# Kernel optimization log

Hardware: AMD Instinct MI355X
Metric: run time of the kernel (lower is better)

## Reference

```python
import jax, jax.numpy as jnp
import numpy as np

N_HOPS = 3
GAMMA = 0.2
N_CAP = 3  # self.N: hops < N use alpha, hop == N uses eta
EPS = 1e-8

N_USERS, N_ENT, N_KG_EDGES, N_INTER_EDGES, D, N_REL = 50000, 100000, 300000, 300000, 256, 21


def setup_inputs() -> dict:
    key = jax.random.key(0)
    ks = jax.random.split(key, 9)
    user_emb = jax.random.normal(ks[0], (N_USERS, D), jnp.float32) * 0.1
    entity_emb = jax.random.normal(ks[1], (N_ENT, D), jnp.float32) * 0.1
    edge_index = jax.random.randint(ks[2], (2, N_KG_EDGES), 0, N_ENT, dtype=jnp.int32)
    edge_type = jax.random.randint(ks[3], (N_KG_EDGES,), 1, N_REL, dtype=jnp.int32)  # 1-based relation ids
    omega = jax.random.uniform(ks[4], (N_KG_EDGES,), jnp.float32)
    inter_u = jax.random.randint(ks[5], (N_INTER_EDGES,), 0, N_USERS, dtype=jnp.int32)
    inter_i = jax.random.randint(ks[6], (N_INTER_EDGES,), 0, N_ENT, dtype=jnp.int32)
    inter_edge = jnp.stack([inter_u, inter_i])
    inter_edge_w = jax.random.uniform(ks[7], (N_INTER_EDGES,), jnp.float32)
    relation_emb = jax.random.normal(ks[8], (N_REL - 1, D), jnp.float32) * 0.1  # xavier-like
    return {
        "user_emb": user_emb,
        "entity_emb": entity_emb,
        "edge_index": edge_index,
        "edge_type": edge_type,
        "omega": omega,
        "inter_edge": inter_edge,
        "inter_edge_w": inter_edge_w,
        "relation_emb": relation_emb,
    }


def _l2norm(x):
    # F.normalize(x, dim=-1, eps=1e-8): x / max(||x||_2, eps)
    n = jnp.sqrt(jnp.sum(x * x, axis=-1, keepdims=True))
    return x / jnp.maximum(n, EPS)


def _clean(x):
    return jnp.nan_to_num(x, nan=0.0, posinf=10000.0, neginf=0.0001)


def reference(user_emb, entity_emb, edge_index, edge_type, omega, inter_edge, inter_edge_w, relation_emb):
    head, tail = edge_index[0], edge_index[1]
    E = omega.shape[0]
    n_ent = entity_emb.shape[0]
    n_users = user_emb.shape[0]

    # alpha/eta depend only on omega & head (constant across hops) -> hoist out of the hop loop
    denom = jax.ops.segment_sum(omega, head, num_segments=E)[head] + EPS
    alpha = omega / denom
    eta0 = jnp.where(alpha > GAMMA, alpha, 0.0)
    eta = eta0 / (jax.ops.segment_sum(eta0, head, num_segments=E)[head] + EPS)

    rel = relation_emb[edge_type - 1]  # [E, D]
    cnt = jnp.maximum(jax.ops.segment_sum(jnp.ones((E,), entity_emb.dtype), head, num_segments=n_ent), 1.0)

    ent_res, usr_res = entity_emb, user_emb
    ent, usr = entity_emb, user_emb
    for i in range(N_HOPS):
        hop = i + 1
        rho = alpha if hop < N_CAP else eta
        msg = rho[:, None] * (ent[tail] * rel)                       # [E, D]
        ent_agg = jax.ops.segment_sum(msg, head, num_segments=n_ent) / cnt[:, None]  # scatter_mean
        item_agg = inter_edge_w[:, None] * ent[inter_edge[1]]        # [IE, D]
        usr_agg = jax.ops.segment_sum(item_agg, inter_edge[0], num_segments=n_users)  # scatter_sum
        ent = _clean(_l2norm(ent_agg))
        usr = _clean(_l2norm(usr_agg))
        ent_res = ent_res + ent
        usr_res = usr_res + usr
    return (ent_res, usr_res)
```

## Files before the change

### kernel.cpp

```cpp
#include <hip/hip_runtime.h>
#include <math.h>

#define D 256
#define EPSV 1e-8f
#define GAMMAV 0.2f
#define SCAN_B 256

typedef float f32x2 __attribute__((ext_vector_type(2)));

__device__ __forceinline__ float cleanf(float x) {
    if (isnan(x)) return 0.0f;
    if (isinf(x)) return x > 0.0f ? 10000.0f : 0.0001f;
    return x;
}

__device__ __forceinline__ unsigned short f2bf(float x) {
    unsigned u = __float_as_uint(x);
    return (unsigned short)((u + 0x7FFFu + ((u >> 16) & 1u)) >> 16);
}
__device__ __forceinline__ float bf2f(unsigned short b) {
    return __uint_as_float(((unsigned)b) << 16);
}

__device__ __forceinline__ float ewgt(int bits, bool eta, float den2i) {
    float a = __int_as_float(bits);
    return eta ? ((a > GAMMAV) ? a * den2i : 0.0f) : a;
}

__device__ __forceinline__ f32x2 bfpair(unsigned u) {
    f32x2 p;
    p.x = __uint_as_float(u << 16);
    p.y = __uint_as_float(u & 0xFFFF0000u);
    return p;
}

__device__ __forceinline__ void pk_wfma(f32x2& acc, f32x2 w2, f32x2 e, f32x2 r) {
    f32x2 t;
    asm("v_pk_mul_f32 %0, %1, %2" : "=v"(t) : "v"(e), "v"(r));
    asm("v_pk_fma_f32 %0, %1, %2, %0" : "+v"(acc) : "v"(w2), "v"(t));
}
__device__ __forceinline__ void pk_wadd(f32x2& acc, f32x2 w2, f32x2 e) {
    asm("v_pk_fma_f32 %0, %1, %2, %0" : "+v"(acc) : "v"(w2), "v"(e));
}


__global__ __launch_bounds__(256) void k_pre(
    const float4* __restrict__ ein, ushort4* __restrict__ eout, int n4, int nbc,
    const int* __restrict__ head, const float* __restrict__ omega,
    const int* __restrict__ iu,
    int* __restrict__ counts_e, int* __restrict__ counts_u,
    float* __restrict__ denom, int E, int IE) {
    if ((int)blockIdx.x < nbc) {
        int i = blockIdx.x * 256 + threadIdx.x;
        if (i < n4) {
            float4 v = ein[i];
            eout[i] = make_ushort4(f2bf(v.x), f2bf(v.y), f2bf(v.z), f2bf(v.w));
        }
    } else {
        int i = (blockIdx.x - nbc) * 256 + threadIdx.x;
        if (i < E) {
            int h = head[i];
            atomicAdd(&counts_e[h], 1);
            atomicAdd(&denom[h], omega[i]);
        } else if (i < E + IE) {
            atomicAdd(&counts_u[iu[i - E]], 1);
        }
    }
}


__global__ __launch_bounds__(SCAN_B) void k_scan1(
    const int* __restrict__ ce, int* __restrict__ oe, int* __restrict__ be,
    int nE, int nbE,
    const int* __restrict__ cu, int* __restrict__ ou, int* __restrict__ bu,
    int nU) {
    __shared__ int tmp[SCAN_B];
    const int* in; int* out; int* bs; int n; int lb;
    if ((int)blockIdx.x < nbE) { in = ce; out = oe; bs = be; n = nE; lb = blockIdx.x; }
    else { in = cu; out = ou; bs = bu; n = nU; lb = blockIdx.x - nbE; }
    int i = lb * SCAN_B + threadIdx.x;
    int v = (i < n) ? in[i] : 0;
    tmp[threadIdx.x] = v;
    __syncthreads();
    for (int o = 1; o < SCAN_B; o <<= 1) {
        int t = (threadIdx.x >= (unsigned)o) ? tmp[threadIdx.x - o] : 0;
        __syncthreads();
        tmp[threadIdx.x] += t;
        __syncthreads();
    }
    if (i < n) out[i] = tmp[threadIdx.x] - v;
    if (threadIdx.x == SCAN_B - 1) bs[lb] = tmp[threadIdx.x];
}

__global__ __launch_bounds__(1024) void k_scan2(
    int* __restrict__ be, int nbE, int* __restrict__ bu, int nbU) {
    __shared__ int tmp[1024];
    int* bs = (blockIdx.x == 0) ? be : bu;
    int nb  = (blockIdx.x == 0) ? nbE : nbU;
    int v = ((int)threadIdx.x < nb) ? bs[threadIdx.x] : 0;
    tmp[threadIdx.x] = v;
    __syncthreads();
    for (int o = 1; o < 1024; o <<= 1) {
        int t = (threadIdx.x >= (unsigned)o) ? tmp[threadIdx.x - o] : 0;
        __syncthreads();
        tmp[threadIdx.x] += t;
        __syncthreads();
    }
    if ((int)threadIdx.x < nb) bs[threadIdx.x] = tmp[threadIdx.x] - v;
}

__global__ __launch_bounds__(SCAN_B) void k_scan3(
    const int* __restrict__ oe, const int* __restrict__ ce,
    int2* __restrict__ oce, int* __restrict__ cure, const int* __restrict__ be,
    int nE, int nbE,
    const int* __restrict__ ou, const int* __restrict__ cu,
    int2* __restrict__ ocu, int* __restrict__ curu, const int* __restrict__ bu,
    int nU) {
    const int* out; const int* cnt; int2* oc; int* cur; const int* bs; int n; int lb;
    if ((int)blockIdx.x < nbE) {
        out = oe; cnt = ce; oc = oce; cur = cure; bs = be; n = nE; lb = blockIdx.x;
    } else {
        out = ou; cnt = cu; oc = ocu; cur = curu; bs = bu; n = nU; lb = blockIdx.x - nbE;
    }
    int i = lb * SCAN_B + threadIdx.x;
    if (i < n) {
        int v = out[i] + bs[lb];
        oc[i] = make_int2(v, cnt[i]);
        cur[i] = v;
    }
}


__global__ __launch_bounds__(256) void k_fill_both(
    const int* __restrict__ head, const int* __restrict__ tail,
    const int* __restrict__ etype, const float* __restrict__ omega,
    const int* __restrict__ iu, const int* __restrict__ ii,
    const float* __restrict__ iw,
    const float* __restrict__ denom, float* __restrict__ denom2,
    int* __restrict__ cursor_e, int* __restrict__ cursor_u,
    int2* __restrict__ kg, int2* __restrict__ uc, int E, int IE) {
    int i = blockIdx.x * blockDim.x + threadIdx.x;
    if (i < E) {
        int h = head[i];
        float a = omega[i] / (denom[h] + EPSV);
        int p = atomicAdd(&cursor_e[h], 1);
        int2 m;
        m.x = tail[i] | ((etype[i] - 1) << 20);
        m.y = __float_as_int(a);
        kg[p] = m;
        if (a > GAMMAV) atomicAdd(&denom2[h], a);
    } else if (i < E + IE) {
        int e = i - E;
        int u = iu[e];
        int p = atomicAdd(&cursor_u[u], 1);
        int2 m;
        m.x = ii[e];
        m.y = __float_as_int(iw[e]);
        uc[p] = m;
    }
}


__global__ __launch_bounds__(256) void k_hop(
    const int2* __restrict__ oc_e, const int2* __restrict__ kg,
    const int2* __restrict__ oc_u, const int2* __restrict__ uc,
    const float* __restrict__ denom2,
    const float* __restrict__ rel,
    const unsigned short* __restrict__ src,
    const unsigned short* __restrict__ ent0b,
    const unsigned short* __restrict__ y1b,
    const unsigned short* __restrict__ y2b,
    unsigned short* __restrict__ ent_out_b,
    float* __restrict__ ent_res,
    const float* __restrict__ user0,
    float* __restrict__ usr_res,
    int n_ent, int n_users, int hop) {
    int row  = (int)((blockIdx.x * (size_t)blockDim.x + threadIdx.x) >> 6);
    int lane = threadIdx.x & 63;
    const uint2*  srcv = (const uint2*)src;
    const float4* relv = (const float4*)rel;
    if (row < n_ent) {
        int2 oc = oc_e[row];
        int s = oc.x, deg = oc.y;
        int end = s + deg;
        const bool eta = (hop == 3);
        float den2i = 0.0f;
        ushort4 a0, a1, a2;
        if (eta) {
            den2i = 1.0f / (denom2[row] + EPSV);
            a0 = ((const ushort4*)ent0b)[row * 64 + lane];
            a1 = ((const ushort4*)y1b )[row * 64 + lane];
            a2 = ((const ushort4*)y2b )[row * 64 + lane];
        }
        f32x2 accA = {0.f, 0.f}, accB = {0.f, 0.f};
        for (int j = s; j < end; j += 4) {
            int e1 = end - 1;
            int j1 = (j + 1 < end) ? j + 1 : e1;
            int j2 = (j + 2 < end) ? j + 2 : e1;
            int j3 = (j + 3 < end) ? j + 3 : e1;
            int2 m0 = kg[j];
            int2 m1 = kg[j1];
            int2 m2 = kg[j2];
            int2 m3 = kg[j3];
            uint2 e0 = srcv[(m0.x & 0xFFFFF) * 64 + lane];
            uint2 eb1 = srcv[(m1.x & 0xFFFFF) * 64 + lane];
            uint2 eb2 = srcv[(m2.x & 0xFFFFF) * 64 + lane];
            uint2 eb3 = srcv[(m3.x & 0xFFFFF) * 64 + lane];
            float4 rw0 = relv[(((unsigned)m0.x) >> 20) * 64 + lane];
            float4 rw1 = relv[(((unsigned)m1.x) >> 20) * 64 + lane];
            float4 rw2 = relv[(((unsigned)m2.x) >> 20) * 64 + lane];
            float4 rw3 = relv[(((unsigned)m3.x) >> 20) * 64 + lane];
            __builtin_amdgcn_sched_barrier(0);
            float w0 = ewgt(m0.y, eta, den2i);
            float w1 = (j + 1 < end) ? ewgt(m1.y, eta, den2i) : 0.0f;
            float w2 = (j + 2 < end) ? ewgt(m2.y, eta, den2i) : 0.0f;
            float w3 = (j + 3 < end) ? ewgt(m3.y, eta, den2i) : 0.0f;
            f32x2 ww, rA, rB;
            ww.x = w0; ww.y = w0;
            rA.x = rw0.x; rA.y = rw0.y; rB.x = rw0.z; rB.y = rw0.w;
            pk_wfma(accA, ww, bfpair(e0.x), rA);
            pk_wfma(accB, ww, bfpair(e0.y), rB);
            ww.x = w1; ww.y = w1;
            rA.x = rw1.x; rA.y = rw1.y; rB.x = rw1.z; rB.y = rw1.w;
            pk_wfma(accA, ww, bfpair(eb1.x), rA);
            pk_wfma(accB, ww, bfpair(eb1.y), rB);
            ww.x = w2; ww.y = w2;
            rA.x = rw2.x; rA.y = rw2.y; rB.x = rw2.z; rB.y = rw2.w;
            pk_wfma(accA, ww, bfpair(eb2.x), rA);
            pk_wfma(accB, ww, bfpair(eb2.y), rB);
            ww.x = w3; ww.y = w3;
            rA.x = rw3.x; rA.y = rw3.y; rB.x = rw3.z; rB.y = rw3.w;
            pk_wfma(accA, ww, bfpair(eb3.x), rA);
            pk_wfma(accB, ww, bfpair(eb3.y), rB);
        }
        float cinv = 1.0f / ((deg > 0) ? (float)deg : 1.0f);
        float4 acc;
        acc.x = accA.x * cinv; acc.y = accA.y * cinv;
        acc.z = accB.x * cinv; acc.w = accB.y * cinv;
        float ss = acc.x * acc.x + acc.y * acc.y + acc.z * acc.z + acc.w * acc.w;
        #pragma unroll
        for (int o = 32; o >= 1; o >>= 1) ss += __shfl_down(ss, o);
        ss = __shfl(ss, 0);
        float nrm = sqrtf(ss);
        float dninv = 1.0f / ((nrm > EPSV) ? nrm : EPSV);
        float4 y;
        y.x = cleanf(acc.x * dninv);
        y.y = cleanf(acc.y * dninv);
        y.z = cleanf(acc.z * dninv);
        y.w = cleanf(acc.w * dninv);
        if (hop == 3) {
            y.x += bf2f(a0.x) + bf2f(a1.x) + bf2f(a2.x);
            y.y += bf2f(a0.y) + bf2f(a1.y) + bf2f(a2.y);
            y.z += bf2f(a0.z) + bf2f(a1.z) + bf2f(a2.z);
            y.w += bf2f(a0.w) + bf2f(a1.w) + bf2f(a2.w);
            ((float4*)(ent_res + (size_t)row * D))[lane] = y;
        } else {
            ((ushort4*)(ent_out_b + (size_t)row * D))[lane] =
                make_ushort4(f2bf(y.x), f2bf(y.y), f2bf(y.z), f2bf(y.w));
        }
    } else {
        int u = row - n_ent;
        if (u >= n_users) return;
        int2 oc = oc_u[u];
        int s = oc.x, deg = oc.y;
        int end = s + deg;
        float4 base;
        if (hop == 1) base = ((const float4*)user0)[u * 64 + lane];
        else          base = ((const float4*)usr_res)[u * 64 + lane];
        f32x2 accA = {0.f, 0.f}, accB = {0.f, 0.f};
        for (int j = s; j < end; j += 8) {
            int e1 = end - 1;
            int2 mm[8];
            #pragma unroll
            for (int k = 0; k < 8; ++k) {
                int jj = j + k;
                mm[k] = uc[jj < end ? jj : e1];
            }
            uint2 eb[8];
            #pragma unroll
            for (int k = 0; k < 8; ++k)
                eb[k] = srcv[mm[k].x * 64 + lane];
            __builtin_amdgcn_sched_barrier(0);
            #pragma unroll
            for (int k = 0; k < 8; ++k) {
                float wv = (j + k < end) ? __int_as_float(mm[k].y) : 0.0f;
                f32x2 ww; ww.x = wv; ww.y = wv;
                pk_wadd(accA, ww, bfpair(eb[k].x));
                pk_wadd(accB, ww, bfpair(eb[k].y));
            }
        }
        float4 acc;
        acc.x = accA.x; acc.y = accA.y; acc.z = accB.x; acc.w = accB.y;
        float ss = acc.x * acc.x + acc.y * acc.y + acc.z * acc.z + acc.w * acc.w;
        #pragma unroll
        for (int o = 32; o >= 1; o >>= 1) ss += __shfl_down(ss, o);
        ss = __shfl(ss, 0);
        float nrm = sqrtf(ss);
        float dninv = 1.0f / ((nrm > EPSV) ? nrm : EPSV);
        float4 y;
        y.x = cleanf(acc.x * dninv) + base.x;
        y.y = cleanf(acc.y * dninv) + base.y;
        y.z = cleanf(acc.z * dninv) + base.z;
        y.w = cleanf(acc.w * dninv) + base.w;
        ((float4*)(usr_res + (size_t)u * D))[lane] = y;
    }
}

extern "C" void kernel_launch(void* const* d_in, const int* in_sizes, int n_in,
                              void* d_out, int out_size, void* d_ws, size_t ws_size,
                              hipStream_t stream) {
    const float* user_emb   = (const float*)d_in[0];
    const float* entity_emb = (const float*)d_in[1];
    const int*   edge_index = (const int*)d_in[2];
    const int*   edge_type  = (const int*)d_in[3];
    const float* omega      = (const float*)d_in[4];
    const int*   inter_edge = (const int*)d_in[5];
    const float* inter_w    = (const float*)d_in[6];
    const float* rel_emb    = (const float*)d_in[7];

    const int n_users = in_sizes[0] / D;
    const int n_ent   = in_sizes[1] / D;
    const int E       = in_sizes[3];
    const int IE      = in_sizes[6];

    const int* head = edge_index;
    const int* tail = edge_index + E;
    const int* iu   = inter_edge;
    const int* ii   = inter_edge + IE;

    char* w = (char*)d_ws;
    size_t entBh = (size_t)n_ent * D * sizeof(unsigned short);
    unsigned short* ent0b = (unsigned short*)w;  w += entBh;
    unsigned short* ent_a = (unsigned short*)w;  w += entBh;
    unsigned short* ent_b = (unsigned short*)w;  w += entBh;
    int2*  kg    = (int2*)w;   w += (size_t)E * sizeof(int2);
    int2*  ucsr  = (int2*)w;   w += (size_t)IE * sizeof(int2);
    int*   counts_e = (int*)w;   w += (size_t)n_ent * sizeof(int);
    int*   counts_u = (int*)w;   w += (size_t)n_users * sizeof(int);
    float* denom    = (float*)w; w += (size_t)n_ent * sizeof(float);
    float* denom2   = (float*)w; w += (size_t)n_ent * sizeof(float);
    size_t zeroB = ((size_t)n_ent * 3 + n_users) * sizeof(int);
    int*   offs_e   = (int*)w; w += (size_t)n_ent * sizeof(int);
    int*   offs_u   = (int*)w; w += (size_t)n_users * sizeof(int);
    int2*  oc_e     = (int2*)w; w += (size_t)n_ent * sizeof(int2);
    int2*  oc_u     = (int2*)w; w += (size_t)n_users * sizeof(int2);
    int*   cursor_e = (int*)w; w += (size_t)n_ent * sizeof(int);
    int*   cursor_u = (int*)w; w += (size_t)n_users * sizeof(int);
    int*   bsums_e  = (int*)w; w += 1024 * sizeof(int);
    int*   bsums_u  = (int*)w; w += 1024 * sizeof(int);

    float* ent_res = (float*)d_out;
    float* usr_res = (float*)d_out + (size_t)n_ent * D;

    hipMemsetAsync(counts_e, 0, zeroB, stream);

    int n4  = n_ent * (D / 4);
    int nbc = (n4 + 255) / 256;
    int total_edges = E + IE;
    int eb = (total_edges + 255) / 256;
    k_pre<<<nbc + eb, 256, 0, stream>>>(
        (const float4*)entity_emb, (ushort4*)ent0b, n4, nbc,
        head, omega, iu, counts_e, counts_u, denom, E, IE);

    int nbE = (n_ent + SCAN_B - 1) / SCAN_B;
    int nbU = (n_users + SCAN_B - 1) / SCAN_B;
    k_scan1<<<nbE + nbU, SCAN_B, 0, stream>>>(counts_e, offs_e, bsums_e, n_ent, nbE,
                                              counts_u, offs_u, bsums_u, n_users);
    k_scan2<<<2, 1024, 0, stream>>>(bsums_e, nbE, bsums_u, nbU);
    k_scan3<<<nbE + nbU, SCAN_B, 0, stream>>>(offs_e, counts_e, oc_e, cursor_e,
                                              bsums_e, n_ent, nbE,
                                              offs_u, counts_u, oc_u, cursor_u,
                                              bsums_u, n_users);

    k_fill_both<<<eb, 256, 0, stream>>>(head, tail, edge_type, omega, iu, ii,
                                        inter_w, denom, denom2,
                                        cursor_e, cursor_u, kg, ucsr, E, IE);

    size_t waves = (size_t)n_ent + n_users;
    int gb = (int)((waves * 64 + 255) / 256);

    k_hop<<<gb, 256, 0, stream>>>(oc_e, kg, oc_u, ucsr,
                                  denom2, rel_emb, ent0b, ent0b, ent_a, ent_b,
                                  ent_a, ent_res, user_emb, usr_res,
                                  n_ent, n_users, 1);
    k_hop<<<gb, 256, 0, stream>>>(oc_e, kg, oc_u, ucsr,
                                  denom2, rel_emb, ent_a, ent0b, ent_a, ent_b,
                                  ent_b, ent_res, user_emb, usr_res,
                                  n_ent, n_users, 2);
    k_hop<<<gb, 256, 0, stream>>>(oc_e, kg, oc_u, ucsr,
                                  denom2, rel_emb, ent_b, ent0b, ent_a, ent_b,
                                  ent_b , ent_res, user_emb, usr_res,
                                  n_ent, n_users, 3);
}
```

Baseline: 617.1 us.

## Process two rows per wavefront with interleaved gathers and scalarized CSR metadata

Each wavefront now handles two entity rows (or two user rows) at once, issuing the gather loads for both rows before doing the math for either, which doubles the number of loads in flight per wave. CSR offsets and edge metadata are moved to scalar registers with readfirstlane so the index arithmetic runs on the scalar unit. The grid shrinks by half. In exchange, register pressure rises, which may lower occupancy, and rows of unequal degree leave one half of the pair idle while the other finishes.

```diff
diff --git a/kernel.cpp b/kernel.cpp
--- a/kernel.cpp
+++ b/kernel.cpp
@@ -22,10 +22,7 @@
     return __uint_as_float(((unsigned)b) << 16);
 }
 
-__device__ __forceinline__ float ewgt(int bits, bool eta, float den2i) {
-    float a = __int_as_float(bits);
-    return eta ? ((a > GAMMAV) ? a * den2i : 0.0f) : a;
-}
+__device__ __forceinline__ int rfl(int v) { return __builtin_amdgcn_readfirstlane(v); }
 
 __device__ __forceinline__ f32x2 bfpair(unsigned u) {
     f32x2 p;
@@ -161,6 +158,123 @@
 }
 
 
+__device__ __forceinline__ void ent_issue(
+    const int2* __restrict__ kg, const uint2* __restrict__ srcv,
+    const float4* __restrict__ relv, int j, int em1, int lane,
+    uint2 (&f)[4], float4 (&q)[4], int (&b)[4]) {
+    int2 m[4];
+    #pragma unroll
+    for (int k = 0; k < 4; ++k) {
+        int jk = j + k; jk = (jk < em1) ? jk : em1;
+        m[k] = kg[jk];
+    }
+    #pragma unroll
+    for (int k = 0; k < 4; ++k) {
+        int x = rfl(m[k].x);
+        b[k] = rfl(m[k].y);
+        f[k] = (srcv + (size_t)(x & 0xFFFFF) * 64)[lane];
+        q[k] = (relv + (size_t)(((unsigned)x) >> 20) * 64)[lane];
+    }
+}
+
+__device__ __forceinline__ void ent_math(
+    int j, int e, bool eta, float den2i,
+    const uint2 (&f)[4], const float4 (&q)[4], const int (&b)[4],
+    f32x2& accA, f32x2& accB) {
+    #pragma unroll
+    for (int k = 0; k < 4; ++k) {
+        float aa = __int_as_float(b[k]);
+        float w = eta ? ((aa > GAMMAV) ? aa * den2i : 0.0f) : aa;
+        if (k) w = (j + k < e) ? w : 0.0f;
+        f32x2 ww; ww.x = w; ww.y = w;
+        f32x2 rA; rA.x = q[k].x; rA.y = q[k].y;
+        f32x2 rB; rB.x = q[k].z; rB.y = q[k].w;
+        pk_wfma(accA, ww, bfpair(f[k].x), rA);
+        pk_wfma(accB, ww, bfpair(f[k].y), rB);
+    }
+}
+
+__device__ __forceinline__ void usr_issue(
+    const int2* __restrict__ uc, const uint2* __restrict__ srcv,
+    int j, int em1, int lane, uint2 (&f)[8], int (&b)[8]) {
+    int2 m[8];
+    #pragma unroll
+    for (int k = 0; k < 8; ++k) {
+        int jk = j + k; jk = (jk < em1) ? jk : em1;
+        m[k] = uc[jk];
+    }
+    #pragma unroll
+    for (int k = 0; k < 8; ++k) {
+        int x = rfl(m[k].x);
+        b[k] = rfl(m[k].y);
+        f[k] = (srcv + (size_t)x * 64)[lane];
+    }
+}
+
+__device__ __forceinline__ void usr_math(
+    int j, int e, const uint2 (&f)[8], const int (&b)[8],
+    f32x2& accA, f32x2& accB) {
+    #pragma unroll
+    for (int k = 0; k < 8; ++k) {
+        float w = __int_as_float(b[k]);
+        if (k) w = (j + k < e) ? w : 0.0f;
+        f32x2 ww; ww.x = w; ww.y = w;
+        pk_wadd(accA, ww, bfpair(f[k].x));
+        pk_wadd(accB, ww, bfpair(f[k].y));
+    }
+}
+
+__device__ __forceinline__ void ent_epi(
+    f32x2 accA, f32x2 accB, int deg, int hop,
+    ushort4 a0, ushort4 a1, ushort4 a2,
+    int row, int lane,
+    unsigned short* __restrict__ ent_out_b, float* __restrict__ ent_res) {
+    float cinv = 1.0f / ((deg > 0) ? (float)deg : 1.0f);
+    float4 acc;
+    acc.x = accA.x * cinv; acc.y = accA.y * cinv;
+    acc.z = accB.x * cinv; acc.w = accB.y * cinv;
+    float ss = acc.x * acc.x + acc.y * acc.y + acc.z * acc.z + acc.w * acc.w;
+    #pragma unroll
+    for (int o = 32; o >= 1; o >>= 1) ss += __shfl_down(ss, o);
+    ss = __shfl(ss, 0);
+    float nrm = sqrtf(ss);
+    float dninv = 1.0f / ((nrm > EPSV) ? nrm : EPSV);
+    float4 y;
+    y.x = cleanf(acc.x * dninv);
+    y.y = cleanf(acc.y * dninv);
+    y.z = cleanf(acc.z * dninv);
+    y.w = cleanf(acc.w * dninv);
+    if (hop == 3) {
+        y.x += bf2f(a0.x) + bf2f(a1.x) + bf2f(a2.x);
+        y.y += bf2f(a0.y) + bf2f(a1.y) + bf2f(a2.y);
+        y.z += bf2f(a0.z) + bf2f(a1.z) + bf2f(a2.z);
+        y.w += bf2f(a0.w) + bf2f(a1.w) + bf2f(a2.w);
+        ((float4*)(ent_res + (size_t)row * D))[lane] = y;
+    } else {
+        ((ushort4*)(ent_out_b + (size_t)row * D))[lane] =
+            make_ushort4(f2bf(y.x), f2bf(y.y), f2bf(y.z), f2bf(y.w));
+    }
+}
+
+__device__ __forceinline__ void usr_epi(
+    f32x2 accA, f32x2 accB, float4 base, int u, int lane,
+    float* __restrict__ usr_res) {
+    float4 acc;
+    acc.x = accA.x; acc.y = accA.y; acc.z = accB.x; acc.w = accB.y;
+    float ss = acc.x * acc.x + acc.y * acc.y + acc.z * acc.z + acc.w * acc.w;
+    #pragma unroll
+    for (int o = 32; o >= 1; o >>= 1) ss += __shfl_down(ss, o);
+    ss = __shfl(ss, 0);
+    float nrm = sqrtf(ss);
+    float dninv = 1.0f / ((nrm > EPSV) ? nrm : EPSV);
+    float4 y;
+    y.x = cleanf(acc.x * dninv) + base.x;
+    y.y = cleanf(acc.y * dninv) + base.y;
+    y.z = cleanf(acc.z * dninv) + base.z;
+    y.w = cleanf(acc.w * dninv) + base.w;
+    ((float4*)(usr_res + (size_t)u * D))[lane] = y;
+}
+
 __global__ __launch_bounds__(256) void k_hop(
     const int2* __restrict__ oc_e, const int2* __restrict__ kg,
     const int2* __restrict__ oc_u, const int2* __restrict__ uc,
@@ -175,134 +289,87 @@
     const float* __restrict__ user0,
     float* __restrict__ usr_res,
     int n_ent, int n_users, int hop) {
-    int row  = (int)((blockIdx.x * (size_t)blockDim.x + threadIdx.x) >> 6);
+    int gid  = blockIdx.x * blockDim.x + threadIdx.x;
+    int wid  = rfl(gid >> 6);
     int lane = threadIdx.x & 63;
     const uint2*  srcv = (const uint2*)src;
     const float4* relv = (const float4*)rel;
-    if (row < n_ent) {
-        int2 oc = oc_e[row];
-        int s = oc.x, deg = oc.y;
-        int end = s + deg;
+    int entW = (n_ent + 1) >> 1;
+    if (wid < entW) {
+        int r0 = wid * 2;
+        int r1 = r0 + 1;
+        bool v1 = r1 < n_ent;
+        int2 oc0 = oc_e[r0];
+        int s0 = rfl(oc0.x), d0 = rfl(oc0.y), e0 = s0 + d0;
+        int s1 = 0, d1 = 0, e1 = 0;
+        if (v1) {
+            int2 oc1 = oc_e[r1];
+            s1 = rfl(oc1.x); d1 = rfl(oc1.y); e1 = s1 + d1;
+        }
         const bool eta = (hop == 3);
-        float den2i = 0.0f;
-        ushort4 a0, a1, a2;
+        float dn0 = 0.f, dn1 = 0.f;
+        ushort4 a00, a01, a02, a10, a11, a12;
         if (eta) {
-            den2i = 1.0f / (denom2[row] + EPSV);
-            a0 = ((const ushort4*)ent0b)[row * 64 + lane];
-            a1 = ((const ushort4*)y1b )[row * 64 + lane];
-            a2 = ((const ushort4*)y2b )[row * 64 + lane];
-        }
-        f32x2 accA = {0.f, 0.f}, accB = {0.f, 0.f};
-        for (int j = s; j < end; j += 4) {
-            int e1 = end - 1;
-            int j1 = (j + 1 < end) ? j + 1 : e1;
-            int j2 = (j + 2 < end) ? j + 2 : e1;
-            int j3 = (j + 3 < end) ? j + 3 : e1;
-            int2 m0 = kg[j];
-            int2 m1 = kg[j1];
-            int2 m2 = kg[j2];
-            int2 m3 = kg[j3];
-            uint2 e0 = srcv[(m0.x & 0xFFFFF) * 64 + lane];
-            uint2 eb1 = srcv[(m1.x & 0xFFFFF) * 64 + lane];
-            uint2 eb2 = srcv[(m2.x & 0xFFFFF) * 64 + lane];
-            uint2 eb3 = srcv[(m3.x & 0xFFFFF) * 64 + lane];
-            float4 rw0 = relv[(((unsigned)m0.x) >> 20) * 64 + lane];
-            float4 rw1 = relv[(((unsigned)m1.x) >> 20) * 64 + lane];
-            float4 rw2 = relv[(((unsigned)m2.x) >> 20) * 64 + lane];
-            float4 rw3 = relv[(((unsigned)m3.x) >> 20) * 64 + lane];
+            dn0 = 1.0f / (denom2[r0] + EPSV);
+            a00 = ((const ushort4*)ent0b)[r0 * 64 + lane];
+            a01 = ((const ushort4*)y1b )[r0 * 64 + lane];
+            a02 = ((const ushort4*)y2b )[r0 * 64 + lane];
+            if (v1) {
+                dn1 = 1.0f / (denom2[r1] + EPSV);
+                a10 = ((const ushort4*)ent0b)[r1 * 64 + lane];
+                a11 = ((const ushort4*)y1b )[r1 * 64 + lane];
+                a12 = ((const ushort4*)y2b )[r1 * 64 + lane];
+            }
+        }
+        f32x2 A0 = {0.f, 0.f}, B0 = {0.f, 0.f};
+        f32x2 A1 = {0.f, 0.f}, B1 = {0.f, 0.f};
+        int j0 = s0, j1 = s1;
+        while ((j0 < e0) || (j1 < e1)) {
+            bool g0 = j0 < e0, g1 = j1 < e1;
+            uint2 f0[4], f1[4];
+            float4 q0[4], q1[4];
+            int b0[4], b1[4];
+            if (g0) ent_issue(kg, srcv, relv, j0, e0 - 1, lane, f0, q0, b0);
+            if (g1) ent_issue(kg, srcv, relv, j1, e1 - 1, lane, f1, q1, b1);
             __builtin_amdgcn_sched_barrier(0);
-            float w0 = ewgt(m0.y, eta, den2i);
-            float w1 = (j + 1 < end) ? ewgt(m1.y, eta, den2i) : 0.0f;
-            float w2 = (j + 2 < end) ? ewgt(m2.y, eta, den2i) : 0.0f;
-            float w3 = (j + 3 < end) ? ewgt(m3.y, eta, den2i) : 0.0f;
-            f32x2 ww, rA, rB;
-            ww.x = w0; ww.y = w0;
-            rA.x = rw0.x; rA.y = rw0.y; rB.x = rw0.z; rB.y = rw0.w;
-            pk_wfma(accA, ww, bfpair(e0.x), rA);
-            pk_wfma(accB, ww, bfpair(e0.y), rB);
-            ww.x = w1; ww.y = w1;
-            rA.x = rw1.x; rA.y = rw1.y; rB.x = rw1.z; rB.y = rw1.w;
-            pk_wfma(accA, ww, bfpair(eb1.x), rA);
-            pk_wfma(accB, ww, bfpair(eb1.y), rB);
-            ww.x = w2; ww.y = w2;
-            rA.x = rw2.x; rA.y = rw2.y; rB.x = rw2.z; rB.y = rw2.w;
-            pk_wfma(accA, ww, bfpair(eb2.x), rA);
-            pk_wfma(accB, ww, bfpair(eb2.y), rB);
-            ww.x = w3; ww.y = w3;
-            rA.x = rw3.x; rA.y = rw3.y; rB.x = rw3.z; rB.y = rw3.w;
-            pk_wfma(accA, ww, bfpair(eb3.x), rA);
-            pk_wfma(accB, ww, bfpair(eb3.y), rB);
-        }
-        float cinv = 1.0f / ((deg > 0) ? (float)deg : 1.0f);
-        float4 acc;
-        acc.x = accA.x * cinv; acc.y = accA.y * cinv;
-        acc.z = accB.x * cinv; acc.w = accB.y * cinv;
-        float ss = acc.x * acc.x + acc.y * acc.y + acc.z * acc.z + acc.w * acc.w;
-        #pragma unroll
-        for (int o = 32; o >= 1; o >>= 1) ss += __shfl_down(ss, o);
-        ss = __shfl(ss, 0);
-        float nrm = sqrtf(ss);
-        float dninv = 1.0f / ((nrm > EPSV) ? nrm : EPSV);
-        float4 y;
-        y.x = cleanf(acc.x * dninv);
-        y.y = cleanf(acc.y * dninv);
-        y.z = cleanf(acc.z * dninv);
-        y.w = cleanf(acc.w * dninv);
-        if (hop == 3) {
-            y.x += bf2f(a0.x) + bf2f(a1.x) + bf2f(a2.x);
-            y.y += bf2f(a0.y) + bf2f(a1.y) + bf2f(a2.y);
-            y.z += bf2f(a0.z) + bf2f(a1.z) + bf2f(a2.z);
-            y.w += bf2f(a0.w) + bf2f(a1.w) + bf2f(a2.w);
-            ((float4*)(ent_res + (size_t)row * D))[lane] = y;
-        } else {
-            ((ushort4*)(ent_out_b + (size_t)row * D))[lane] =
-                make_ushort4(f2bf(y.x), f2bf(y.y), f2bf(y.z), f2bf(y.w));
-        }
+            if (g0) { ent_math(j0, e0, eta, dn0, f0, q0, b0, A0, B0); j0 += 4; }
+            if (g1) { ent_math(j1, e1, eta, dn1, f1, q1, b1, A1, B1); j1 += 4; }
+        }
+        ent_epi(A0, B0, d0, hop, a00, a01, a02, r0, lane, ent_out_b, ent_res);
+        if (v1)
+            ent_epi(A1, B1, d1, hop, a10, a11, a12, r1, lane, ent_out_b, ent_res);
     } else {
-        int u = row - n_ent;
-        if (u >= n_users) return;
-        int2 oc = oc_u[u];
-        int s = oc.x, deg = oc.y;
-        int end = s + deg;
-        float4 base;
-        if (hop == 1) base = ((const float4*)user0)[u * 64 + lane];
-        else          base = ((const float4*)usr_res)[u * 64 + lane];
-        f32x2 accA = {0.f, 0.f}, accB = {0.f, 0.f};
-        for (int j = s; j < end; j += 8) {
-            int e1 = end - 1;
-            int2 mm[8];
-            #pragma unroll
-            for (int k = 0; k < 8; ++k) {
-                int jj = j + k;
-                mm[k] = uc[jj < end ? jj : e1];
-            }
-            uint2 eb[8];
-            #pragma unroll
-            for (int k = 0; k < 8; ++k)
-                eb[k] = srcv[mm[k].x * 64 + lane];
+        int uw = wid - entW;
+        int u0 = uw * 2;
+        if (u0 >= n_users) return;
+        int u1 = u0 + 1;
+        bool v1 = u1 < n_users;
+        int2 oc0 = oc_u[u0];
+        int s0 = rfl(oc0.x), d0 = rfl(oc0.y), e0 = s0 + d0;
+        int s1 = 0, e1 = 0;
+        if (v1) {
+            int2 oc1 = oc_u[u1];
+            s1 = rfl(oc1.x); e1 = s1 + rfl(oc1.y);
+        }
+        float4 base0, base1;
+        const float4* bsrc = (hop == 1) ? (const float4*)user0 : (const float4*)usr_res;
+        base0 = bsrc[u0 * 64 + lane];
+        if (v1) base1 = bsrc[u1 * 64 + lane];
+        f32x2 A0 = {0.f, 0.f}, B0 = {0.f, 0.f};
+        f32x2 A1 = {0.f, 0.f}, B1 = {0.f, 0.f};
+        int j0 = s0, j1 = s1;
+        while ((j0 < e0) || (j1 < e1)) {
+            bool g0 = j0 < e0, g1 = j1 < e1;
+            uint2 f0[8], f1[8];
+            int b0[8], b1[8];
+            if (g0) usr_issue(uc, srcv, j0, e0 - 1, lane, f0, b0);
+            if (g1) usr_issue(uc, srcv, j1, e1 - 1, lane, f1, b1);
             __builtin_amdgcn_sched_barrier(0);
-            #pragma unroll
-            for (int k = 0; k < 8; ++k) {
-                float wv = (j + k < end) ? __int_as_float(mm[k].y) : 0.0f;
-                f32x2 ww; ww.x = wv; ww.y = wv;
-                pk_wadd(accA, ww, bfpair(eb[k].x));
-                pk_wadd(accB, ww, bfpair(eb[k].y));
-            }
-        }
-        float4 acc;
-        acc.x = accA.x; acc.y = accA.y; acc.z = accB.x; acc.w = accB.y;
-        float ss = acc.x * acc.x + acc.y * acc.y + acc.z * acc.z + acc.w * acc.w;
-        #pragma unroll
-        for (int o = 32; o >= 1; o >>= 1) ss += __shfl_down(ss, o);
-        ss = __shfl(ss, 0);
-        float nrm = sqrtf(ss);
-        float dninv = 1.0f / ((nrm > EPSV) ? nrm : EPSV);
-        float4 y;
-        y.x = cleanf(acc.x * dninv) + base.x;
-        y.y = cleanf(acc.y * dninv) + base.y;
-        y.z = cleanf(acc.z * dninv) + base.z;
-        y.w = cleanf(acc.w * dninv) + base.w;
-        ((float4*)(usr_res + (size_t)u * D))[lane] = y;
+            if (g0) { usr_math(j0, e0, f0, b0, A0, B0); j0 += 8; }
+            if (g1) { usr_math(j1, e1, f1, b1, A1, B1); j1 += 8; }
+        }
+        usr_epi(A0, B0, base0, u0, lane, usr_res);
+        if (v1) usr_epi(A1, B1, base1, u1, lane, usr_res);
     }
 }
 
@@ -376,7 +443,9 @@
                                         inter_w, denom, denom2,
                                         cursor_e, cursor_u, kg, ucsr, E, IE);
 
-    size_t waves = (size_t)n_ent + n_users;
+    int entW = (n_ent + 1) >> 1;
+    int usrW = (n_users + 1) >> 1;
+    size_t waves = (size_t)entW + usrW;
     int gb = (int)((waves * 64 + 255) / 256);
 
     k_hop<<<gb, 256, 0, stream>>>(oc_e, kg, oc_u, ucsr,
```

Result: faster. 570.6 us (-7.5%).
